# Kernel tuning notes

Measured on AMD Instinct MI355X. Metric: run time of the kernel, lower is better.

## Reference

```python
import jax, jax.numpy as jnp
import numpy as np

N_TOKENS = 8192
D_MODEL = 1024
N_EXPERT = 8
TOP_K = 2
D_HIDDEN = 4 * D_MODEL


def setup_inputs() -> dict:
    key = jax.random.key(0)
    ks = jax.random.split(key, 7)
    s_in = 1.0 / np.sqrt(D_MODEL)
    s_hid = 1.0 / np.sqrt(D_HIDDEN)
    return {
        "inp": jax.random.normal(ks[0], (N_TOKENS, D_MODEL), dtype=jnp.float32),
        "gate_w": jax.random.normal(ks[1], (D_MODEL, N_EXPERT), dtype=jnp.float32) * s_in,
        "gate_b": jnp.zeros((N_EXPERT,), dtype=jnp.float32),
        "w1": jax.random.normal(ks[2], (N_EXPERT, D_MODEL, D_HIDDEN), dtype=jnp.float32) * s_in,
        "b1": jnp.zeros((N_EXPERT, D_HIDDEN), dtype=jnp.float32),
        "w2": jax.random.normal(ks[3], (N_EXPERT, D_HIDDEN, D_MODEL), dtype=jnp.float32) * s_hid,
        "b2": jnp.zeros((N_EXPERT, D_MODEL), dtype=jnp.float32),
    }


def reference(inp, gate_w, gate_b, w1, b1, w2, b2):
    # NaiveGate: linear logits -> top_k -> softmax over the selected k logits
    logits = inp @ gate_w + gate_b                      # [N, E]
    top_vals, top_idx = jax.lax.top_k(logits, TOP_K)    # [N, K]
    gate_score = jax.nn.softmax(top_vals, axis=-1)      # [N, K]

    # Dispatch/combine: y[n] = sum_k score[n,k] * expert_{idx[n,k]}(x[n]).
    # Loop over the small fixed expert set; mask-weighted accumulate replaces
    # the scatter / grouped-GEMM / gather of the original (same math).
    y = jnp.zeros_like(inp)
    for e in range(N_EXPERT):
        h = jax.nn.gelu(inp @ w1[e] + b1[e])             # [N, H]
        o = h @ w2[e] + b2[e]                            # [N, D]
        w_e = jnp.sum(gate_score * (top_idx == e), axis=-1)  # [N]
        y = y + w_e[:, None] * o
    return y
```

## Files before the change

kernel.cpp:

```cpp
#include <hip/hip_runtime.h>
#include <hip/hip_bf16.h>

#define NT 8192
#define DM 1024
#define NE 8
#define DH 4096
#define NP (NT * 2)

typedef __attribute__((ext_vector_type(8))) __bf16 bf16x8;
typedef __attribute__((ext_vector_type(4))) float f32x4;

__device__ __forceinline__ ushort f2bf(float f) {
  unsigned int x = __float_as_uint(f);
  unsigned int r = (x + 0x7fffu + ((x >> 16) & 1u)) >> 16;
  return (ushort)r;
}

__device__ __forceinline__ float gelu_fast(float x) {
  float x2 = x * x;
  float t = __builtin_fmaf(x2, 0.044715f, 1.0f);
  float m = x * t * 2.3025851f;
  m = fminf(m, 126.0f);
  float p = __builtin_amdgcn_exp2f(m);
  return x * p * __builtin_amdgcn_rcpf(p + 1.0f);
}

__device__ __forceinline__ void async_copy16(const void* gsrc, void* ldst) {
  __builtin_amdgcn_global_load_lds(
      (const __attribute__((address_space(1))) void*)gsrc,
      (__attribute__((address_space(3))) void*)ldst, 16, 0, 0);
}

__global__ __launch_bounds__(256) void transpose2_kernel(
    const float* __restrict__ w1, const float* __restrict__ w2,
    ushort* __restrict__ w1t, ushort* __restrict__ w2t) {
  const int b = blockIdx.x;
  const int which = b >> 13;
  const int rem = b & 8191;
  const int e = rem >> 10;
  const int t = rem & 1023;
  const float* src;
  ushort* dst;
  int R, C, c0, r0;
  if (which == 0) {
    src = w1 + (size_t)e * DM * DH; dst = w1t + (size_t)e * DM * DH;
    R = DM; C = DH; c0 = (t & 63) * 64; r0 = (t >> 6) * 64;
  } else {
    src = w2 + (size_t)e * DM * DH; dst = w2t + (size_t)e * DM * DH;
    R = DH; C = DM; c0 = (t & 15) * 64; r0 = (t >> 4) * 64;
  }
  __shared__ ushort tileT[64][72];
  const int tx = threadIdx.x & 15, ty = threadIdx.x >> 4;
#pragma unroll
  for (int i = 0; i < 4; i++) {
    int r = ty + i * 16;
    float4 v = *(const float4*)(src + (size_t)(r0 + r) * C + c0 + tx * 4);
    tileT[tx * 4 + 0][r] = f2bf(v.x);
    tileT[tx * 4 + 1][r] = f2bf(v.y);
    tileT[tx * 4 + 2][r] = f2bf(v.z);
    tileT[tx * 4 + 3][r] = f2bf(v.w);
  }
  __syncthreads();
#pragma unroll
  for (int i = 0; i < 4; i++) {
    int c = ty + i * 16;
    *(ushort4*)(dst + (size_t)(c0 + c) * R + r0 + tx * 4) = *(const ushort4*)(&tileT[c][tx * 4]);
  }
}

__global__ void gate_cvt_kernel(const float* __restrict__ inp, const float* __restrict__ gw,
                                const float* __restrict__ gb, ushort* __restrict__ inp_bf,
                                int* __restrict__ counts, int* __restrict__ tok_list,
                                float* __restrict__ scale_list, int* __restrict__ pair_loc) {
  int wave = threadIdx.x >> 6, lane = threadIdx.x & 63;
  int token = blockIdx.x * 4 + wave;
  const float* x = inp + (size_t)token * DM;
  ushort* xb = inp_bf + (size_t)token * DM;
  float acc[NE];
#pragma unroll
  for (int e = 0; e < NE; e++) acc[e] = 0.f;
#pragma unroll
  for (int j = 0; j < 16; j++) {
    int idx = j * 64 + lane;
    float xv = x[idx];
    xb[idx] = f2bf(xv);
    const float4* g = (const float4*)(gw + (size_t)idx * NE);
    float4 g0 = g[0], g1 = g[1];
    acc[0] += xv * g0.x; acc[1] += xv * g0.y; acc[2] += xv * g0.z; acc[3] += xv * g0.w;
    acc[4] += xv * g1.x; acc[5] += xv * g1.y; acc[6] += xv * g1.z; acc[7] += xv * g1.w;
  }
#pragma unroll
  for (int e = 0; e < NE; e++) {
    for (int off = 32; off; off >>= 1) acc[e] += __shfl_xor(acc[e], off, 64);
  }
  if (lane == 0) {
    float v[NE];
#pragma unroll
    for (int e = 0; e < NE; e++) v[e] = acc[e] + gb[e];
    int i0 = 0; float b0 = v[0];
#pragma unroll
    for (int e = 1; e < NE; e++) if (v[e] > b0) { b0 = v[e]; i0 = e; }
    int i1 = -1; float b1v = -INFINITY;
#pragma unroll
    for (int e = 0; e < NE; e++) if (e != i0 && v[e] > b1v) { b1v = v[e]; i1 = e; }
    float s1 = 1.f / (1.f + __expf(b0 - b1v));
    float s0 = 1.f - s1;
    int p0 = atomicAdd(&counts[i0], 1);
    tok_list[i0 * NT + p0] = token;
    scale_list[i0 * NT + p0] = s0;
    pair_loc[token * 2 + 0] = i0 * NT + p0;
    int p1 = atomicAdd(&counts[i1], 1);
    tok_list[i1 * NT + p1] = token;
    scale_list[i1 * NT + p1] = s1;
    pair_loc[token * 2 + 1] = i1 * NT + p1;
  }
}


#define STAGE_TILE(base)                                      \
  do {                                                        \
    async_copy16(aP0, (char*)(base) + wv * 1024);             \
    async_copy16(aP1, (char*)(base) + 4096 + wv * 1024);      \
    async_copy16(bP0, (char*)(base) + 8192 + wv * 1024);      \
    async_copy16(bP1, (char*)(base) + 12288 + wv * 1024);     \
    aP0 += 32; aP1 += 32; bP0 += 32; bP1 += 32;               \
  } while (0)

__global__ __launch_bounds__(256) void gemm1_kernel(
    const ushort* __restrict__ xbf, const ushort* __restrict__ w1t,
    const float* __restrict__ b1, const int* __restrict__ tok_list,
    const int* __restrict__ counts, ushort* __restrict__ hbuf) {
  const int b = blockIdx.x;
  const int e = b & 7;
  const int idx = b >> 3;
  const int mTile = idx & 63;
  const int nTile = idx >> 6;
  int off = 0;
  for (int i = 0; i < e; i++) off += counts[i];
  const int cnt = counts[e];
  if (mTile * 128 >= cnt) return;

  __shared__ __attribute__((aligned(128))) char ldsB[49152];

  const int t = threadIdx.x;
  const int lane = t & 63, wv = t >> 6;
  const int wm = wv & 1, wn = wv >> 1;

  const int sr = t >> 2;
  const int sc = (((t & 3) ^ ((sr >> 1) & 3)) * 8);
  int gi0 = mTile * 128 + sr;      if (gi0 >= cnt) gi0 = cnt - 1;
  int gi1 = mTile * 128 + 64 + sr; if (gi1 >= cnt) gi1 = cnt - 1;
  const int tok0 = tok_list[e * NT + gi0];
  const int tok1 = tok_list[e * NT + gi1];
  const ushort* aP0 = xbf + (size_t)tok0 * DM + sc;
  const ushort* aP1 = xbf + (size_t)tok1 * DM + sc;
  const ushort* bP0 = w1t + ((size_t)e * DH + nTile * 128 + sr) * DM + sc;
  const ushort* bP1 = bP0 + (size_t)64 * DM;

  f32x4 zero = {0.f, 0.f, 0.f, 0.f};
  f32x4 acc[4][4];
#pragma unroll
  for (int i = 0; i < 4; i++)
#pragma unroll
    for (int j = 0; j < 4; j++) acc[i][j] = zero;

  const int quad = lane >> 4, lc = lane & 15;
  const int rq = quad ^ ((lc >> 1) & 3);

  auto compute = [&](const char* buf) {
    const char* A_ = buf;
    const char* B_ = buf + 8192;
    bf16x8 af[4], bfr[4];
#pragma unroll
    for (int mi = 0; mi < 4; mi++) {
      int row = wm * 64 + mi * 16 + lc;
      af[mi] = *(const bf16x8*)(A_ + row * 64 + rq * 16);
    }
#pragma unroll
    for (int ni = 0; ni < 4; ni++) {
      int row = wn * 64 + ni * 16 + lc;
      bfr[ni] = *(const bf16x8*)(B_ + row * 64 + rq * 16);
    }
#pragma unroll
    for (int mi = 0; mi < 4; mi++)
#pragma unroll
      for (int ni = 0; ni < 4; ni++)
        acc[mi][ni] = __builtin_amdgcn_mfma_f32_16x16x32_bf16(af[mi], bfr[ni], acc[mi][ni], 0, 0, 0);
  };

  const int NIT = DM / 32;
  STAGE_TILE(ldsB);
  STAGE_TILE(ldsB + 16384);
  int cur = 0;
  for (int tt = 0; tt < NIT - 1; ++tt) {
    asm volatile("s_waitcnt vmcnt(4)" ::: "memory");
    __builtin_amdgcn_s_barrier();
    if (tt + 2 < NIT) {
      int nx = cur + 2; if (nx >= 3) nx -= 3;
      STAGE_TILE(ldsB + nx * 16384);
    }
    compute(ldsB + cur * 16384);
    cur = (cur == 2) ? 0 : cur + 1;
  }
  asm volatile("s_waitcnt vmcnt(0)" ::: "memory");
  __builtin_amdgcn_s_barrier();
  compute(ldsB + cur * 16384);

  float bias[4];
#pragma unroll
  for (int ni = 0; ni < 4; ni++)
    bias[ni] = b1[(size_t)e * DH + nTile * 128 + wn * 64 + ni * 16 + lc];

#pragma unroll
  for (int mi = 0; mi < 4; mi++) {
#pragma unroll
    for (int r = 0; r < 4; r++) {
      int lr = wm * 64 + mi * 16 + quad * 4 + r;
      int gi = mTile * 128 + lr;
      if (gi < cnt) {
        ushort* hrow = hbuf + (size_t)(off + gi) * DH + nTile * 128 + wn * 64 + lc;
#pragma unroll
        for (int ni = 0; ni < 4; ni++) {
          float v = acc[mi][ni][r] + bias[ni];
          hrow[ni * 16] = f2bf(gelu_fast(v));
        }
      }
    }
  }
}

__global__ __launch_bounds__(256) void gemm2_kernel(
    const ushort* __restrict__ hbuf, const ushort* __restrict__ w2t,
    const float* __restrict__ b2, const int* __restrict__ counts,
    float* __restrict__ pbuf) {
  const int b = blockIdx.x;
  const int e = b & 7;
  const int idx = b >> 3;
  const int nTile = idx & 7;
  const int mTile = idx >> 3;
  int off = 0;
  for (int i = 0; i < e; i++) off += counts[i];
  const int cnt = counts[e];
  if (mTile * 128 >= cnt) return;

  __shared__ __attribute__((aligned(128))) char ldsB[49152];

  const int t = threadIdx.x;
  const int lane = t & 63, wv = t >> 6;
  const int wm = wv & 1, wn = wv >> 1;

  const int sr = t >> 2;
  const int sc = (((t & 3) ^ ((sr >> 1) & 3)) * 8);
  int gi0 = mTile * 128 + sr;      if (gi0 >= cnt) gi0 = cnt - 1;
  int gi1 = mTile * 128 + 64 + sr; if (gi1 >= cnt) gi1 = cnt - 1;
  const ushort* aP0 = hbuf + (size_t)(off + gi0) * DH + sc;
  const ushort* aP1 = hbuf + (size_t)(off + gi1) * DH + sc;
  const ushort* bP0 = w2t + ((size_t)e * DM + nTile * 128 + sr) * DH + sc;
  const ushort* bP1 = bP0 + (size_t)64 * DH;

  f32x4 zero = {0.f, 0.f, 0.f, 0.f};
  f32x4 acc[4][4];
#pragma unroll
  for (int i = 0; i < 4; i++)
#pragma unroll
    for (int j = 0; j < 4; j++) acc[i][j] = zero;

  const int quad = lane >> 4, lc = lane & 15;
  const int rq = quad ^ ((lc >> 1) & 3);

  auto compute = [&](const char* buf) {
    const char* A_ = buf;
    const char* B_ = buf + 8192;
    bf16x8 af[4], bfr[4];
#pragma unroll
    for (int mi = 0; mi < 4; mi++) {
      int row = wm * 64 + mi * 16 + lc;
      af[mi] = *(const bf16x8*)(A_ + row * 64 + rq * 16);
    }
#pragma unroll
    for (int ni = 0; ni < 4; ni++) {
      int row = wn * 64 + ni * 16 + lc;
      bfr[ni] = *(const bf16x8*)(B_ + row * 64 + rq * 16);
    }
#pragma unroll
    for (int mi = 0; mi < 4; mi++)
#pragma unroll
      for (int ni = 0; ni < 4; ni++)
        acc[mi][ni] = __builtin_amdgcn_mfma_f32_16x16x32_bf16(af[mi], bfr[ni], acc[mi][ni], 0, 0, 0);
  };

  const int NIT = DH / 32;
  STAGE_TILE(ldsB);
  STAGE_TILE(ldsB + 16384);
  int cur = 0;
  for (int tt = 0; tt < NIT - 1; ++tt) {
    asm volatile("s_waitcnt vmcnt(4)" ::: "memory");
    __builtin_amdgcn_s_barrier();
    if (tt + 2 < NIT) {
      int nx = cur + 2; if (nx >= 3) nx -= 3;
      STAGE_TILE(ldsB + nx * 16384);
    }
    compute(ldsB + cur * 16384);
    cur = (cur == 2) ? 0 : cur + 1;
  }
  asm volatile("s_waitcnt vmcnt(0)" ::: "memory");
  __builtin_amdgcn_s_barrier();
  compute(ldsB + cur * 16384);

  float bias[4];
#pragma unroll
  for (int ni = 0; ni < 4; ni++)
    bias[ni] = b2[(size_t)e * DM + nTile * 128 + wn * 64 + ni * 16 + lc];

#pragma unroll
  for (int mi = 0; mi < 4; mi++) {
#pragma unroll
    for (int r = 0; r < 4; r++) {
      int lr = wm * 64 + mi * 16 + quad * 4 + r;
      int gi = mTile * 128 + lr;
      if (gi < cnt) {
        float* prow = pbuf + (size_t)(off + gi) * DM + nTile * 128 + wn * 64 + lc;
#pragma unroll
        for (int ni = 0; ni < 4; ni++)
          prow[ni * 16] = acc[mi][ni][r] + bias[ni];
      }
    }
  }
}

__global__ __launch_bounds__(256) void combine_kernel(
    const float* __restrict__ pbuf, const int* __restrict__ pair_loc,
    const float* __restrict__ scale_list, const int* __restrict__ counts,
    float* __restrict__ y) {
  const int wave = threadIdx.x >> 6, lane = threadIdx.x & 63;
  const int tk = blockIdx.x * 4 + wave;
  const int loc0 = pair_loc[tk * 2 + 0];
  const int loc1 = pair_loc[tk * 2 + 1];
  const float s0 = scale_list[loc0];
  const float s1 = scale_list[loc1];
  const int e0 = loc0 >> 13, p0 = loc0 & (NT - 1);
  const int e1 = loc1 >> 13, p1 = loc1 & (NT - 1);
  int r0 = p0, r1 = p1;
#pragma unroll
  for (int i = 0; i < NE; i++) {
    int c = counts[i];
    if (i < e0) r0 += c;
    if (i < e1) r1 += c;
  }
  const float4* a = (const float4*)(pbuf + (size_t)r0 * DM) + lane;
  const float4* bq = (const float4*)(pbuf + (size_t)r1 * DM) + lane;
  float4* yo = (float4*)(y + (size_t)tk * DM) + lane;
#pragma unroll
  for (int j = 0; j < 4; j++) {
    float4 av = a[j * 64], bv = bq[j * 64];
    float4 o;
    o.x = s0 * av.x + s1 * bv.x;
    o.y = s0 * av.y + s1 * bv.y;
    o.z = s0 * av.z + s1 * bv.z;
    o.w = s0 * av.w + s1 * bv.w;
    yo[j * 64] = o;
  }
}

extern "C" void kernel_launch(void* const* d_in, const int* in_sizes, int n_in,
                              void* d_out, int out_size, void* d_ws, size_t ws_size,
                              hipStream_t stream) {
  const float* inp = (const float*)d_in[0];
  const float* gw  = (const float*)d_in[1];
  const float* gb  = (const float*)d_in[2];
  const float* w1  = (const float*)d_in[3];
  const float* b1  = (const float*)d_in[4];
  const float* w2  = (const float*)d_in[5];
  const float* b2  = (const float*)d_in[6];
  float* y = (float*)d_out;

  char* ws = (char*)d_ws;
  ushort* inp_bf = (ushort*)ws;              ws += (size_t)NT * DM * 2;
  ushort* w1t    = (ushort*)ws;              ws += (size_t)NE * DH * DM * 2;
  ushort* w2t    = (ushort*)ws;              ws += (size_t)NE * DM * DH * 2;
  ushort* hbuf   = (ushort*)ws;              ws += (size_t)NP * DH * 2;
  int*    tok_list   = (int*)ws;             ws += (size_t)NE * NT * 4;
  float*  scale_list = (float*)ws;           ws += (size_t)NE * NT * 4;
  int*    counts     = (int*)ws;             ws += 256;
  int*    pair_loc   = (int*)ws;             ws += (size_t)NT * 2 * 4;

  float* pbuf = (float*)w1t;

  hipMemsetAsync(counts, 0, 256, stream);

  transpose2_kernel<<<2 * NE * 1024, 256, 0, stream>>>(w1, w2, w1t, w2t);
  gate_cvt_kernel<<<NT / 4, 256, 0, stream>>>(inp, gw, gb, inp_bf, counts, tok_list, scale_list, pair_loc);
  gemm1_kernel<<<NE * 32 * 64, 256, 0, stream>>>(inp_bf, w1t, b1, tok_list, counts, hbuf);
  gemm2_kernel<<<NE * 8 * 64, 256, 0, stream>>>(hbuf, w2t, b2, counts, pbuf);
  combine_kernel<<<NT / 4, 256, 0, stream>>>(pbuf, pair_loc, scale_list, counts, y);
}
```

Measured before the change: 916.3 us.

## Fuse combine into gemm2 via atomic scatter-add and merge pre-kernels

Weight transpose, gating/conversion and zeroing of the output are merged into one launch. The separate combine kernel is removed: gemm2 scales its results by the gate score and atomically adds them into y at the token row. This drops the fp32 pbuf write and re-read along with two launches, at the cost of float atomics on y and a summation order that is no longer deterministic.

```diff
diff --git a/kernel.cpp b/kernel.cpp
--- a/kernel.cpp
+++ b/kernel.cpp
@@ -31,88 +31,95 @@
       (__attribute__((address_space(3))) void*)ldst, 16, 0, 0);
 }
 
-__global__ __launch_bounds__(256) void transpose2_kernel(
+__global__ __launch_bounds__(256) void fused_pre_kernel(
     const float* __restrict__ w1, const float* __restrict__ w2,
-    ushort* __restrict__ w1t, ushort* __restrict__ w2t) {
+    ushort* __restrict__ w1t, ushort* __restrict__ w2t,
+    const float* __restrict__ inp, const float* __restrict__ gw,
+    const float* __restrict__ gb, ushort* __restrict__ inp_bf,
+    int* __restrict__ counts, int* __restrict__ tok_list,
+    float* __restrict__ scale_list, float* __restrict__ y) {
+  __shared__ ushort tileT[64][72];
   const int b = blockIdx.x;
-  const int which = b >> 13;
-  const int rem = b & 8191;
-  const int e = rem >> 10;
-  const int t = rem & 1023;
-  const float* src;
-  ushort* dst;
-  int R, C, c0, r0;
-  if (which == 0) {
-    src = w1 + (size_t)e * DM * DH; dst = w1t + (size_t)e * DM * DH;
-    R = DM; C = DH; c0 = (t & 63) * 64; r0 = (t >> 6) * 64;
+
+  if (b < 16384) {
+    const int which = b >> 13;
+    const int rem = b & 8191;
+    const int e = rem >> 10;
+    const int t = rem & 1023;
+    const float* src;
+    ushort* dst;
+    int R, C, c0, r0;
+    if (which == 0) {
+      src = w1 + (size_t)e * DM * DH; dst = w1t + (size_t)e * DM * DH;
+      R = DM; C = DH; c0 = (t & 63) * 64; r0 = (t >> 6) * 64;
+    } else {
+      src = w2 + (size_t)e * DM * DH; dst = w2t + (size_t)e * DM * DH;
+      R = DH; C = DM; c0 = (t & 15) * 64; r0 = (t >> 4) * 64;
+    }
+    const int tx = threadIdx.x & 15, ty = threadIdx.x >> 4;
+#pragma unroll
+    for (int i = 0; i < 4; i++) {
+      int r = ty + i * 16;
+      float4 v = *(const float4*)(src + (size_t)(r0 + r) * C + c0 + tx * 4);
+      tileT[tx * 4 + 0][r] = f2bf(v.x);
+      tileT[tx * 4 + 1][r] = f2bf(v.y);
+      tileT[tx * 4 + 2][r] = f2bf(v.z);
+      tileT[tx * 4 + 3][r] = f2bf(v.w);
+    }
+    __syncthreads();
+#pragma unroll
+    for (int i = 0; i < 4; i++) {
+      int c = ty + i * 16;
+      *(ushort4*)(dst + (size_t)(c0 + c) * R + r0 + tx * 4) = *(const ushort4*)(&tileT[c][tx * 4]);
+    }
+  } else if (b < 18432) {
+    const int wave = threadIdx.x >> 6, lane = threadIdx.x & 63;
+    const int token = (b - 16384) * 4 + wave;
+    const float* x = inp + (size_t)token * DM;
+    ushort* xb = inp_bf + (size_t)token * DM;
+    float acc[NE];
+#pragma unroll
+    for (int e = 0; e < NE; e++) acc[e] = 0.f;
+#pragma unroll
+    for (int j = 0; j < 16; j++) {
+      int idx = j * 64 + lane;
+      float xv = x[idx];
+      xb[idx] = f2bf(xv);
+      const float4* g = (const float4*)(gw + (size_t)idx * NE);
+      float4 g0 = g[0], g1 = g[1];
+      acc[0] += xv * g0.x; acc[1] += xv * g0.y; acc[2] += xv * g0.z; acc[3] += xv * g0.w;
+      acc[4] += xv * g1.x; acc[5] += xv * g1.y; acc[6] += xv * g1.z; acc[7] += xv * g1.w;
+    }
+#pragma unroll
+    for (int e = 0; e < NE; e++) {
+      for (int off = 32; off; off >>= 1) acc[e] += __shfl_xor(acc[e], off, 64);
+    }
+    if (lane == 0) {
+      float v[NE];
+#pragma unroll
+      for (int e = 0; e < NE; e++) v[e] = acc[e] + gb[e];
+      int i0 = 0; float b0 = v[0];
+#pragma unroll
+      for (int e = 1; e < NE; e++) if (v[e] > b0) { b0 = v[e]; i0 = e; }
+      int i1 = -1; float b1v = -INFINITY;
+#pragma unroll
+      for (int e = 0; e < NE; e++) if (e != i0 && v[e] > b1v) { b1v = v[e]; i1 = e; }
+      float s1 = 1.f / (1.f + __expf(b0 - b1v));
+      float s0 = 1.f - s1;
+      int p0 = atomicAdd(&counts[i0], 1);
+      tok_list[i0 * NT + p0] = token;
+      scale_list[i0 * NT + p0] = s0;
+      int p1 = atomicAdd(&counts[i1], 1);
+      tok_list[i1 * NT + p1] = token;
+      scale_list[i1 * NT + p1] = s1;
+    }
   } else {
-    src = w2 + (size_t)e * DM * DH; dst = w2t + (size_t)e * DM * DH;
-    R = DH; C = DM; c0 = (t & 15) * 64; r0 = (t >> 4) * 64;
-  }
-  __shared__ ushort tileT[64][72];
-  const int tx = threadIdx.x & 15, ty = threadIdx.x >> 4;
-#pragma unroll
-  for (int i = 0; i < 4; i++) {
-    int r = ty + i * 16;
-    float4 v = *(const float4*)(src + (size_t)(r0 + r) * C + c0 + tx * 4);
-    tileT[tx * 4 + 0][r] = f2bf(v.x);
-    tileT[tx * 4 + 1][r] = f2bf(v.y);
-    tileT[tx * 4 + 2][r] = f2bf(v.z);
-    tileT[tx * 4 + 3][r] = f2bf(v.w);
-  }
-  __syncthreads();
-#pragma unroll
-  for (int i = 0; i < 4; i++) {
-    int c = ty + i * 16;
-    *(ushort4*)(dst + (size_t)(c0 + c) * R + r0 + tx * 4) = *(const ushort4*)(&tileT[c][tx * 4]);
-  }
-}
-
-__global__ void gate_cvt_kernel(const float* __restrict__ inp, const float* __restrict__ gw,
-                                const float* __restrict__ gb, ushort* __restrict__ inp_bf,
-                                int* __restrict__ counts, int* __restrict__ tok_list,
-                                float* __restrict__ scale_list, int* __restrict__ pair_loc) {
-  int wave = threadIdx.x >> 6, lane = threadIdx.x & 63;
-  int token = blockIdx.x * 4 + wave;
-  const float* x = inp + (size_t)token * DM;
-  ushort* xb = inp_bf + (size_t)token * DM;
-  float acc[NE];
-#pragma unroll
-  for (int e = 0; e < NE; e++) acc[e] = 0.f;
-#pragma unroll
-  for (int j = 0; j < 16; j++) {
-    int idx = j * 64 + lane;
-    float xv = x[idx];
-    xb[idx] = f2bf(xv);
-    const float4* g = (const float4*)(gw + (size_t)idx * NE);
-    float4 g0 = g[0], g1 = g[1];
-    acc[0] += xv * g0.x; acc[1] += xv * g0.y; acc[2] += xv * g0.z; acc[3] += xv * g0.w;
-    acc[4] += xv * g1.x; acc[5] += xv * g1.y; acc[6] += xv * g1.z; acc[7] += xv * g1.w;
-  }
-#pragma unroll
-  for (int e = 0; e < NE; e++) {
-    for (int off = 32; off; off >>= 1) acc[e] += __shfl_xor(acc[e], off, 64);
-  }
-  if (lane == 0) {
-    float v[NE];
-#pragma unroll
-    for (int e = 0; e < NE; e++) v[e] = acc[e] + gb[e];
-    int i0 = 0; float b0 = v[0];
-#pragma unroll
-    for (int e = 1; e < NE; e++) if (v[e] > b0) { b0 = v[e]; i0 = e; }
-    int i1 = -1; float b1v = -INFINITY;
-#pragma unroll
-    for (int e = 0; e < NE; e++) if (e != i0 && v[e] > b1v) { b1v = v[e]; i1 = e; }
-    float s1 = 1.f / (1.f + __expf(b0 - b1v));
-    float s0 = 1.f - s1;
-    int p0 = atomicAdd(&counts[i0], 1);
-    tok_list[i0 * NT + p0] = token;
-    scale_list[i0 * NT + p0] = s0;
-    pair_loc[token * 2 + 0] = i0 * NT + p0;
-    int p1 = atomicAdd(&counts[i1], 1);
-    tok_list[i1 * NT + p1] = token;
-    scale_list[i1 * NT + p1] = s1;
-    pair_loc[token * 2 + 1] = i1 * NT + p1;
+    const int idx = b - 18432;
+    float4* dst = (float4*)(y + (size_t)idx * 4096);
+    f32x4 z = {0.f, 0.f, 0.f, 0.f};
+#pragma unroll
+    for (int j = 0; j < 4; j++)
+      ((f32x4*)dst)[j * 256 + threadIdx.x] = z;
   }
 }
 
@@ -231,8 +238,9 @@
 
 __global__ __launch_bounds__(256) void gemm2_kernel(
     const ushort* __restrict__ hbuf, const ushort* __restrict__ w2t,
-    const float* __restrict__ b2, const int* __restrict__ counts,
-    float* __restrict__ pbuf) {
+    const float* __restrict__ b2, const int* __restrict__ tok_list,
+    const float* __restrict__ scale_list, const int* __restrict__ counts,
+    float* __restrict__ y) {
   const int b = blockIdx.x;
   const int e = b & 7;
   const int idx = b >> 3;
@@ -319,46 +327,16 @@
       int lr = wm * 64 + mi * 16 + quad * 4 + r;
       int gi = mTile * 128 + lr;
       if (gi < cnt) {
-        float* prow = pbuf + (size_t)(off + gi) * DM + nTile * 128 + wn * 64 + lc;
-#pragma unroll
-        for (int ni = 0; ni < 4; ni++)
-          prow[ni * 16] = acc[mi][ni][r] + bias[ni];
+        int tok = tok_list[e * NT + gi];
+        float s = scale_list[e * NT + gi];
+        float* yrow = y + (size_t)tok * DM + nTile * 128 + wn * 64 + lc;
+#pragma unroll
+        for (int ni = 0; ni < 4; ni++) {
+          float v = (acc[mi][ni][r] + bias[ni]) * s;
+          unsafeAtomicAdd(&yrow[ni * 16], v);
+        }
       }
     }
-  }
-}
-
-__global__ __launch_bounds__(256) void combine_kernel(
-    const float* __restrict__ pbuf, const int* __restrict__ pair_loc,
-    const float* __restrict__ scale_list, const int* __restrict__ counts,
-    float* __restrict__ y) {
-  const int wave = threadIdx.x >> 6, lane = threadIdx.x & 63;
-  const int tk = blockIdx.x * 4 + wave;
-  const int loc0 = pair_loc[tk * 2 + 0];
-  const int loc1 = pair_loc[tk * 2 + 1];
-  const float s0 = scale_list[loc0];
-  const float s1 = scale_list[loc1];
-  const int e0 = loc0 >> 13, p0 = loc0 & (NT - 1);
-  const int e1 = loc1 >> 13, p1 = loc1 & (NT - 1);
-  int r0 = p0, r1 = p1;
-#pragma unroll
-  for (int i = 0; i < NE; i++) {
-    int c = counts[i];
-    if (i < e0) r0 += c;
-    if (i < e1) r1 += c;
-  }
-  const float4* a = (const float4*)(pbuf + (size_t)r0 * DM) + lane;
-  const float4* bq = (const float4*)(pbuf + (size_t)r1 * DM) + lane;
-  float4* yo = (float4*)(y + (size_t)tk * DM) + lane;
-#pragma unroll
-  for (int j = 0; j < 4; j++) {
-    float4 av = a[j * 64], bv = bq[j * 64];
-    float4 o;
-    o.x = s0 * av.x + s1 * bv.x;
-    o.y = s0 * av.y + s1 * bv.y;
-    o.z = s0 * av.z + s1 * bv.z;
-    o.w = s0 * av.w + s1 * bv.w;
-    yo[j * 64] = o;
   }
 }
 
@@ -382,15 +360,11 @@
   int*    tok_list   = (int*)ws;             ws += (size_t)NE * NT * 4;
   float*  scale_list = (float*)ws;           ws += (size_t)NE * NT * 4;
   int*    counts     = (int*)ws;             ws += 256;
-  int*    pair_loc   = (int*)ws;             ws += (size_t)NT * 2 * 4;
-
-  float* pbuf = (float*)w1t;
 
   hipMemsetAsync(counts, 0, 256, stream);
 
-  transpose2_kernel<<<2 * NE * 1024, 256, 0, stream>>>(w1, w2, w1t, w2t);
-  gate_cvt_kernel<<<NT / 4, 256, 0, stream>>>(inp, gw, gb, inp_bf, counts, tok_list, scale_list, pair_loc);
+  fused_pre_kernel<<<20480, 256, 0, stream>>>(w1, w2, w1t, w2t, inp, gw, gb,
+                                              inp_bf, counts, tok_list, scale_list, y);
   gemm1_kernel<<<NE * 32 * 64, 256, 0, stream>>>(inp_bf, w1t, b1, tok_list, counts, hbuf);
-  gemm2_kernel<<<NE * 8 * 64, 256, 0, stream>>>(hbuf, w2t, b2, counts, pbuf);
-  combine_kernel<<<NT / 4, 256, 0, stream>>>(pbuf, pair_loc, scale_list, counts, y);
-}
+  gemm2_kernel<<<NE * 8 * 64, 256, 0, stream>>>(hbuf, w2t, b2, tok_list, scale_list, counts, y);
+}
```

Result: no change. 905.6 us (-1.2%).
